# Kernel tuning notes

Hardware: AMD Instinct MI355X
Metric: run time of the kernel (lower is better)

## Reference

```python
import jax, jax.numpy as jnp
import numpy as np

B, S, D, H = 4, 2048, 1024, 16
HD = D // H  # 64

def setup_inputs() -> dict:
    key = jax.random.key(0)
    ks = jax.random.split(key, 6)
    scale = 1.0 / np.sqrt(D)
    return {
        "x": jax.random.normal(ks[0], (B, S, D), dtype=jnp.float32),
        "Wq": jax.random.normal(ks[1], (D, D), dtype=jnp.float32) * scale,
        "Wk": jax.random.normal(ks[2], (D, D), dtype=jnp.float32) * scale,
        "Wv": jax.random.normal(ks[3], (D, D), dtype=jnp.float32) * scale,
        "Wo": jax.random.normal(ks[4], (D, D), dtype=jnp.float32) * scale,
        "bo": jnp.zeros((D,), dtype=jnp.float32),
    }

def reference(x, Wq, Wk, Wv, Wo, bo):
    b, s, d = x.shape
    # projections (no bias for q/k/v, matching QKV_BIAS=False)
    q = (x @ Wq).reshape(b, s, H, HD).transpose(0, 2, 1, 3)  # [b,h,s,hd]
    k = (x @ Wk).reshape(b, s, H, HD).transpose(0, 2, 1, 3)
    v = (x @ Wv).reshape(b, s, H, HD).transpose(0, 2, 1, 3)
    scores = jnp.einsum('bhqd,bhkd->bhqk', q, k)  # [b,h,s,s]
    causal = jnp.tril(jnp.ones((s, s), dtype=bool))  # True where allowed
    scores = jnp.where(causal, scores, -jnp.inf)
    attn = jax.nn.softmax(scores / np.sqrt(HD), axis=-1)
    ctx = jnp.einsum('bhqk,bhkd->bhqd', attn, v)  # [b,h,s,hd]
    ctx = ctx.transpose(0, 2, 1, 3).reshape(b, s, d)
    return ctx @ Wo + bo
```

## Files before the change

kernel.cpp:

```cpp
#include <hip/hip_runtime.h>

#define BSZ 4
#define SEQ 2048
#define DIM 1024
#define NH  16
#define HD  64
#define QT  128
#define KT  64
#define PAD 72
#define NKT (DIM / 64)

typedef float v4f __attribute__((ext_vector_type(4)));
typedef short s8v __attribute__((ext_vector_type(8)));
typedef unsigned short u16;
typedef unsigned short u16x8 __attribute__((ext_vector_type(8)));
typedef unsigned short u16x4 __attribute__((ext_vector_type(4)));
typedef unsigned int u32;
typedef unsigned int u32x2 __attribute__((ext_vector_type(2)));
typedef unsigned int u32x4 __attribute__((ext_vector_type(4)));

__device__ __forceinline__ u16 f2bf(float f) {
  u32 u = __builtin_bit_cast(u32, f);
  u32 r = u + 0x7fffu + ((u >> 16) & 1u);
  return (u16)(r >> 16);
}
__device__ __forceinline__ u32 cvtpk(float lo, float hi) {
  u32 r; asm("v_cvt_pk_bf16_f32 %0, %1, %2" : "=v"(r) : "v"(lo), "v"(hi)); return r;
}
__device__ __forceinline__ u16 f2bf1(float f) { return (u16)cvtpk(f, f); }
__device__ __forceinline__ float fast_exp2(float x) {
#if __has_builtin(__builtin_amdgcn_exp2f)
  return __builtin_amdgcn_exp2f(x);
#else
  return exp2f(x);
#endif
}
__device__ __forceinline__ void gll16(const u16* g, u16* l) {
  __builtin_amdgcn_global_load_lds((const __attribute__((address_space(1))) void*)g,
                                   (__attribute__((address_space(3))) void*)l, 16, 0, 0);
}
__device__ __forceinline__ void wg_barrier() { asm volatile("s_barrier" ::: "memory"); }
#define WAITCNT_LGKM0 0xC07F
#define VMW6 __builtin_amdgcn_s_waitcnt(0xF76);
#define VMW0 __builtin_amdgcn_s_waitcnt(0xF70);

__global__ __launch_bounds__(256) void cast_bf16_kernel(const float* __restrict__ x,
                                                        u16* __restrict__ o, int n4) {
  int i = blockIdx.x * 256 + threadIdx.x;
  if (i >= n4) return;
  v4f v = reinterpret_cast<const v4f*>(x)[i];
  u16x4 r;
  #pragma unroll
  for (int c = 0; c < 4; c++) r[c] = f2bf(v[c]);
  reinterpret_cast<u16x4*>(o)[i] = r;
}

__global__ __launch_bounds__(256) void transpose_cast_kernel(const float* __restrict__ W0,
                                                             const float* __restrict__ W1,
                                                             const float* __restrict__ W2,
                                                             const float* __restrict__ W3,
                                                             u16* __restrict__ out) {
  const float* W = blockIdx.z == 0 ? W0 : blockIdx.z == 1 ? W1 : blockIdx.z == 2 ? W2 : W3;
  const float scale = (blockIdx.z == 0) ? 0.18033688011112042f : 1.0f;
  u16* T = out + (size_t)blockIdx.z * DIM * DIM;
  __shared__ float tile[32][33];
  int tx = threadIdx.x & 31, ty = threadIdx.x >> 5;
  int bn = blockIdx.x * 32, bk = blockIdx.y * 32;
  #pragma unroll
  for (int r = 0; r < 4; r++) {
    int k = bk + ty + r * 8;
    tile[ty + r * 8][tx] = W[(size_t)k * DIM + bn + tx];
  }
  __syncthreads();
  #pragma unroll
  for (int r = 0; r < 4; r++) {
    int n = bn + ty + r * 8;
    T[(size_t)n * DIM + bk + tx] = f2bf(tile[tx][ty + r * 8] * scale);
  }
}


#define ST_TILE(t_, s_)                                                           \
  gll16(Ag0 + (t_) * 64,      AW0 + (s_) * 16384);                                \
  gll16(Ag1 + (t_) * 64,      AW1 + (s_) * 16384);                                \
  gll16(Ag0 + (t_) * 64 + 32, AW0 + (s_) * 16384 + 8192);                         \
  gll16(Ag1 + (t_) * 64 + 32, AW1 + (s_) * 16384 + 8192);                         \
  gll16(Bg0 + (t_) * 64,      BW0 + (s_) * 8192);                                 \
  gll16(Bg0 + (t_) * 64 + 32, BW0 + (s_) * 8192 + 4096);

#define PH(t_, s_, STAGES, VMW)                                                   \
  { const u16* Ab = AL + (s_) * 16384 + aRd;                                      \
    const u16* Bb = BL + (s_) * 8192 + bRd;                                       \
    s8v af[2][4], bf[2][4];                                                       \
    _Pragma("unroll") for (int kc_ = 0; kc_ < 2; kc_++) {                         \
      _Pragma("unroll") for (int i_ = 0; i_ < 4; i_++)                            \
        af[kc_][i_] = *(const s8v*)(Ab + kc_ * 8192 + i_ * 512);                  \
      _Pragma("unroll") for (int j_ = 0; j_ < 4; j_++)                            \
        bf[kc_][j_] = *(const s8v*)(Bb + kc_ * 4096 + j_ * 512);                  \
    }                                                                             \
    STAGES                                                                        \
    VMW                                                                           \
    wg_barrier();                                                                 \
    __builtin_amdgcn_s_waitcnt(WAITCNT_LGKM0);                                    \
    __builtin_amdgcn_s_setprio(1);                                                \
    _Pragma("unroll") for (int kc_ = 0; kc_ < 2; kc_++)                           \
      _Pragma("unroll") for (int i_ = 0; i_ < 4; i_++)                            \
        _Pragma("unroll") for (int j_ = 0; j_ < 4; j_++)                          \
          acc[i_][j_] = __builtin_amdgcn_mfma_f32_16x16x32_bf16(                  \
              af[kc_][i_], bf[kc_][j_], acc[i_][j_], 0, 0, 0);                    \
    __builtin_amdgcn_s_setprio(0);                                                \
    wg_barrier(); }

#define GEMM256x128_CORE()                                                        \
  extern __shared__ __align__(16) u16 lds[];                                      \
  const int t = threadIdx.x;                                                      \
  const int lane = t & 63, w = t >> 6;                                            \
  const int waveM = w >> 1, waveN = w & 1;                                        \
  const int quad = lane >> 4, l16 = lane & 15;                                    \
  const int sR = lane & 15, sC = lane >> 4;                                       \
  u16* AL = lds;                                                                  \
  u16* BL = lds + 49152;                                                          \
  v4f acc[4][4];                                                                  \
  _Pragma("unroll") for (int i = 0; i < 4; i++)                                   \
    _Pragma("unroll") for (int j = 0; j < 4; j++)                                 \
      acc[i][j] = (v4f){0.f, 0.f, 0.f, 0.f};                                      \
  const u16* Ag0 = A + (size_t)(m0 + w * 32 + sR) * DIM + sC * 8;                 \
  const u16* Ag1 = Ag0 + 16 * DIM;                                                \
  const u16* Bg0 = Bt + (size_t)(n0 + w * 16 + sR) * DIM + sC * 8;                \
  u16* AW0 = AL + w * 1024;                                                       \
  u16* AW1 = AL + w * 1024 + 512;                                                 \
  u16* BW0 = BL + w * 512;                                                        \
  const int aRd = waveM * 2048 + quad * 128 + l16 * 8;                            \
  const int bRd = waveN * 2048 + quad * 128 + l16 * 8;                            \
  ST_TILE(0, 0) ST_TILE(1, 1)                                                     \
  VMW6                                                                            \
  wg_barrier();                                                                   \
  _Pragma("unroll") for (int t3 = 0; t3 < 12; t3 += 3) {                          \
    PH(t3 + 0, 0, ST_TILE(t3 + 2, 2), VMW6)                                       \
    PH(t3 + 1, 1, ST_TILE(t3 + 3, 0), VMW6)                                       \
    PH(t3 + 2, 2, ST_TILE(t3 + 4, 1), VMW6)                                       \
  }                                                                               \
  PH(12, 0, ST_TILE(14, 2), VMW6)                                                 \
  PH(13, 1, ST_TILE(15, 0), VMW6)                                                 \
  PH(14, 2, , VMW0)                                                               \
  PH(15, 0, , )

__global__ __launch_bounds__(512, 2) void gemm_qkv(const u16* __restrict__ A, const u16* __restrict__ Wt,
                                                   u16* __restrict__ Qb, u16* __restrict__ Kb,
                                                   u16* __restrict__ Vtg) {
  const int bid = blockIdx.x;
  const int swz = (bid & 7) * 96 + (bid >> 3);
  const int z = swz >> 8;
  const int rem = swz & 255;
  const int m0 = (rem >> 3) * 256;
  const int n0 = (rem & 7) * 128;
  const u16* Bt = Wt + (size_t)z * DIM * DIM;
  GEMM256x128_CORE()
  if (z == 2) {
    #pragma unroll
    for (int mi = 0; mi < 4; mi++) {
      #pragma unroll
      for (int ni = 0; ni < 4; ni++) {
        int gm0 = m0 + waveM * 64 + mi * 16 + quad * 4;
        int gn = n0 + waveN * 64 + ni * 16 + l16;
        int b = gm0 >> 11, s0 = gm0 & (SEQ - 1), hh = gn >> 6, d = gn & (HD - 1);
        u32x2 pw;
        pw[0] = cvtpk(acc[mi][ni][0], acc[mi][ni][1]);
        pw[1] = cvtpk(acc[mi][ni][2], acc[mi][ni][3]);
        *(u16x4*)(Vtg + ((size_t)(b * NH + hh) * HD + d) * SEQ + s0) =
            __builtin_bit_cast(u16x4, pw);
      }
    }
  } else {
    u16* C = (z == 0) ? Qb : Kb;
    #pragma unroll
    for (int mi = 0; mi < 4; mi++) {
      #pragma unroll
      for (int ni = 0; ni < 4; ni++) {
        int gn = n0 + waveN * 64 + ni * 16 + l16;
        #pragma unroll
        for (int r = 0; r < 4; r++) {
          int gm = m0 + waveM * 64 + mi * 16 + quad * 4 + r;
          C[(size_t)gm * DIM + gn] = f2bf1(acc[mi][ni][r]);
        }
      }
    }
  }
}

__global__ __launch_bounds__(512, 2) void gemm_proj(const u16* __restrict__ A, const u16* __restrict__ Bt,
                                                    float* __restrict__ Cf, const float* __restrict__ bias) {
  const int bid = blockIdx.x;
  const int swz = (bid & 7) * 32 + (bid >> 3);
  const int m0 = (swz >> 3) * 256;
  const int n0 = (swz & 7) * 128;
  GEMM256x128_CORE()
  #pragma unroll
  for (int ni = 0; ni < 4; ni++) {
    int gn = n0 + waveN * 64 + ni * 16 + l16;
    float bv = bias[gn];
    #pragma unroll
    for (int mi = 0; mi < 4; mi++) {
      #pragma unroll
      for (int r = 0; r < 4; r++) {
        int gm = m0 + waveM * 64 + mi * 16 + quad * 4 + r;
        Cf[(size_t)gm * DIM + gn] = acc[mi][ni][r] + bv;
      }
    }
  }
}

__global__ __launch_bounds__(256, 3) void flash_attn_mfma(const u16* __restrict__ Qb,
                                                          const u16* __restrict__ Kb,
                                                          const u16* __restrict__ Vtg,
                                                          u16* __restrict__ Ob) {
  const int h = blockIdx.x, px = blockIdx.y, bb = blockIdx.z;
  const int t = threadIdx.x;
  const int lane = t & 63, w = t >> 6;
  const int quad = lane >> 4, l16 = lane & 15;

  __shared__ u16 QPs[QT * PAD];
  __shared__ u16 Ks[KT * PAD];
  __shared__ u16 Vs[HD * PAD];

  const size_t qkbase = (size_t)bb * SEQ * DIM + h * HD;
  const size_t vbase = ((size_t)bb * NH + h) * (size_t)HD * SEQ;

  const int vrow = t >> 2, scol = (t & 3) * 16;
  const int krow = ((vrow >> 5) + 2 * ((vrow >> 2) & 1)) * 16 + ((vrow >> 3) & 3) * 4 + (vrow & 3);

  for (int pass = 0; pass < 2; pass++) {
    const int qi = (pass == 0) ? px : (SEQ / QT - 1 - px);
    const int q0 = qi * QT;
    const int wq = q0 + w * 32;
    const int ntiles = 2 * qi + 2;

    __syncthreads();

    {
      const int r = t >> 1, c0 = (t & 1) * 32;
      const u16* src = Qb + qkbase + (size_t)(q0 + r) * DIM + c0;
      #pragma unroll
      for (int ch = 0; ch < 4; ch++)
        *(u16x8*)(QPs + r * PAD + c0 + ch * 8) = *(const u16x8*)(src + ch * 8);
    }
    __syncthreads();

    s8v qf[2][2];
    #pragma unroll
    for (int ni = 0; ni < 2; ni++)
      #pragma unroll
      for (int kc = 0; kc < 2; kc++)
        qf[ni][kc] = *(const s8v*)(QPs + (w * 32 + ni * 16 + l16) * PAD + kc * 32 + quad * 8);

    u16x8 kr0, kr1, vr0, vr1;
    {
      const u16* kp = Kb + qkbase + (size_t)vrow * DIM + scol;
      kr0 = *(const u16x8*)kp; kr1 = *(const u16x8*)(kp + 8);
      const u16* vp = Vtg + vbase + (size_t)vrow * SEQ + scol;
      vr0 = *(const u16x8*)vp; vr1 = *(const u16x8*)(vp + 8);
    }

    float mrun[2] = {-1e30f, -1e30f}, lrun[2] = {0.f, 0.f};
    v4f O[4][2];
    #pragma unroll
    for (int di = 0; di < 4; di++)
      #pragma unroll
      for (int ni = 0; ni < 2; ni++) O[di][ni] = (v4f){0.f, 0.f, 0.f, 0.f};

    for (int it = 0; it < ntiles; ++it) {
      const int kv0 = it * KT;
      __syncthreads();
      *(u16x8*)(Ks + krow * PAD + scol) = kr0;
      *(u16x8*)(Ks + krow * PAD + scol + 8) = kr1;
      *(u16x8*)(Vs + vrow * PAD + scol) = vr0;
      *(u16x8*)(Vs + vrow * PAD + scol + 8) = vr1;
      __syncthreads();
      if (it + 1 < ntiles) {
        const int nkv = kv0 + KT;
        const u16* kp = Kb + qkbase + (size_t)(nkv + vrow) * DIM + scol;
        kr0 = *(const u16x8*)kp; kr1 = *(const u16x8*)(kp + 8);
        const u16* vp = Vtg + vbase + (size_t)vrow * SEQ + nkv + scol;
        vr0 = *(const u16x8*)vp; vr1 = *(const u16x8*)(vp + 8);
      }
      if (kv0 > wq + 31) continue;

      v4f sc[4][2];
      #pragma unroll
      for (int mi = 0; mi < 4; mi++)
        #pragma unroll
        for (int ni = 0; ni < 2; ni++) sc[mi][ni] = (v4f){0.f, 0.f, 0.f, 0.f};
      #pragma unroll
      for (int kc = 0; kc < 2; kc++) {
        #pragma unroll
        for (int mi = 0; mi < 4; mi++) {
          s8v kf = *(const s8v*)(Ks + (mi * 16 + l16) * PAD + kc * 32 + quad * 8);
          sc[mi][0] = __builtin_amdgcn_mfma_f32_16x16x32_bf16(kf, qf[0][kc], sc[mi][0], 0, 0, 0);
          sc[mi][1] = __builtin_amdgcn_mfma_f32_16x16x32_bf16(kf, qf[1][kc], sc[mi][1], 0, 0, 0);
        }
      }

      if (kv0 + KT > wq) {
        #pragma unroll
        for (int mi = 0; mi < 4; mi++) {
          const int kvb = kv0 + (mi & 1) * 32 + quad * 8 + (mi >> 1) * 4;
          #pragma unroll
          for (int ni = 0; ni < 2; ni++) {
            const int qg = wq + ni * 16 + l16;
            #pragma unroll
            for (int r = 0; r < 4; r++)
              if (kvb + r > qg) sc[mi][ni][r] = -1e30f;
          }
        }
      }

      float mx[2];
      #pragma unroll
      for (int ni = 0; ni < 2; ni++) {
        float m = -1e30f;
        #pragma unroll
        for (int mi = 0; mi < 4; mi++)
          #pragma unroll
          for (int r = 0; r < 4; r++) m = fmaxf(m, sc[mi][ni][r]);
        m = fmaxf(m, __shfl_xor(m, 16, 64));
        m = fmaxf(m, __shfl_xor(m, 32, 64));
        mx[ni] = m;
      }
      const bool defer = __all((mx[0] <= mrun[0] + 8.f) && (mx[1] <= mrun[1] + 8.f));
      if (!defer) {
        float alpha[2];
        #pragma unroll
        for (int ni = 0; ni < 2; ni++) {
          const float mnew = fmaxf(mrun[ni], mx[ni]);
          alpha[ni] = fast_exp2(mrun[ni] - mnew);
          mrun[ni] = mnew;
          lrun[ni] *= alpha[ni];
        }
        #pragma unroll
        for (int di = 0; di < 4; di++)
          #pragma unroll
          for (int ni = 0; ni < 2; ni++)
            #pragma unroll
            for (int r = 0; r < 4; r++) O[di][ni][r] *= alpha[ni];
      }
      #pragma unroll
      for (int ni = 0; ni < 2; ni++) {
        float rsum = 0.f;
        #pragma unroll
        for (int mi = 0; mi < 4; mi++)
          #pragma unroll
          for (int r = 0; r < 4; r++) {
            float p = fast_exp2(sc[mi][ni][r] - mrun[ni]);
            sc[mi][ni][r] = p;
            rsum += p;
          }
        rsum += __shfl_xor(rsum, 16, 64);
        rsum += __shfl_xor(rsum, 32, 64);
        lrun[ni] += rsum;
      }

      s8v pf[2][2];
      #pragma unroll
      for (int ni = 0; ni < 2; ni++)
        #pragma unroll
        for (int kc = 0; kc < 2; kc++) {
          u32x4 wds;
          wds[0] = cvtpk(sc[kc][ni][0], sc[kc][ni][1]);
          wds[1] = cvtpk(sc[kc][ni][2], sc[kc][ni][3]);
          wds[2] = cvtpk(sc[kc + 2][ni][0], sc[kc + 2][ni][1]);
          wds[3] = cvtpk(sc[kc + 2][ni][2], sc[kc + 2][ni][3]);
          pf[ni][kc] = __builtin_bit_cast(s8v, wds);
        }

      #pragma unroll
      for (int kc = 0; kc < 2; kc++) {
        #pragma unroll
        for (int di = 0; di < 4; di++) {
          s8v vf = *(const s8v*)(Vs + (di * 16 + l16) * PAD + kc * 32 + quad * 8);
          O[di][0] = __builtin_amdgcn_mfma_f32_16x16x32_bf16(vf, pf[0][kc], O[di][0], 0, 0, 0);
          O[di][1] = __builtin_amdgcn_mfma_f32_16x16x32_bf16(vf, pf[1][kc], O[di][1], 0, 0, 0);
        }
      }
    }

    const float inv0 = 1.f / lrun[0], inv1 = 1.f / lrun[1];
    #pragma unroll
    for (int di = 0; di < 4; di++)
      #pragma unroll
      for (int ni = 0; ni < 2; ni++) {
        const float inv = ni ? inv1 : inv0;
        #pragma unroll
        for (int r = 0; r < 4; r++)
          QPs[(w * 32 + ni * 16 + l16) * PAD + di * 16 + quad * 4 + r] = f2bf1(O[di][ni][r] * inv);
      }
    __syncthreads();
    {
      const int r = t >> 1, c0 = (t & 1) * 32;
      u16* dst = Ob + qkbase + (size_t)(q0 + r) * DIM + c0;
      #pragma unroll
      for (int ch = 0; ch < 4; ch++)
        *(u16x8*)(dst + ch * 8) = *(const u16x8*)(QPs + r * PAD + c0 + ch * 8);
    }
  }
}

extern "C" void kernel_launch(void* const* d_in, const int* in_sizes, int n_in,
                              void* d_out, int out_size, void* d_ws, size_t ws_size,
                              hipStream_t stream) {
  (void)in_sizes; (void)n_in; (void)out_size; (void)ws_size;
  const float* x  = (const float*)d_in[0];
  const float* Wq = (const float*)d_in[1];
  const float* Wk = (const float*)d_in[2];
  const float* Wv = (const float*)d_in[3];
  const float* Wo = (const float*)d_in[4];
  const float* bo = (const float*)d_in[5];
  float* out = (float*)d_out;

  static bool lds_attr_done = false;
  if (!lds_attr_done) {
    hipFuncSetAttribute(reinterpret_cast<const void*>(gemm_qkv),
                        hipFuncAttributeMaxDynamicSharedMemorySize, 147456);
    hipFuncSetAttribute(reinterpret_cast<const void*>(gemm_proj),
                        hipFuncAttributeMaxDynamicSharedMemorySize, 147456);
    lds_attr_done = true;
  }

  char* ws = (char*)d_ws;
  const size_t MB = 1024ull * 1024ull;
  u16* Xb  = (u16*)(ws);
  u16* Wt  = (u16*)(ws + 16 * MB);
  u16* Qb  = (u16*)(ws + 24 * MB);
  u16* Kb  = (u16*)(ws + 40 * MB);
  u16* Vtg = (u16*)(ws + 56 * MB);
  u16* Cb  = (u16*)(ws + 72 * MB);

  const int NTOK = BSZ * SEQ;
  const int n4 = NTOK * DIM / 4;
  cast_bf16_kernel<<<(n4 + 255) / 256, 256, 0, stream>>>(x, Xb, n4);
  transpose_cast_kernel<<<dim3(32, 32, 4), 256, 0, stream>>>(Wq, Wk, Wv, Wo, Wt);

  gemm_qkv<<<dim3(768), 512, 147456, stream>>>(Xb, Wt, Qb, Kb, Vtg);

  flash_attn_mfma<<<dim3(NH, SEQ / QT / 2, BSZ), 256, 0, stream>>>(Qb, Kb, Vtg, Cb);

  gemm_proj<<<dim3(256), 512, 147456, stream>>>(Cb, Wt + 3ull * DIM * DIM, out, bo);
}
```

Before: 266.2 us.

## Software-pipeline LDS fragment loads with MFMA in GEMM core via half-k double buffering

Restructures the GEMM main loop so each 64-wide k tile is split into two halves with separate register fragment sets (A/B). LDS reads for the next half are issued before the MFMAs on the current half run, with partial lgkmcnt waits and scheduling barriers. Global-to-LDS staging for the next tile also overlaps with compute, and the loop uses one barrier per tile instead of two. The cost is more live fragment registers, which could affect occupancy under the 512x2 launch bounds, plus a VMW0 wait each tile that may expose global load latency.

```diff
diff --git a/kernel.cpp b/kernel.cpp
--- a/kernel.cpp
+++ b/kernel.cpp
@@ -41,8 +41,10 @@
 }
 __device__ __forceinline__ void wg_barrier() { asm volatile("s_barrier" ::: "memory"); }
 #define WAITCNT_LGKM0 0xC07F
+#define WAITCNT_LGKM8 0xC87F
 #define VMW6 __builtin_amdgcn_s_waitcnt(0xF76);
 #define VMW0 __builtin_amdgcn_s_waitcnt(0xF70);
+#define SCHEDB __builtin_amdgcn_sched_barrier(0);
 
 __global__ __launch_bounds__(256) void cast_bf16_kernel(const float* __restrict__ x,
                                                         u16* __restrict__ o, int n4) {
@@ -88,28 +90,38 @@
   gll16(Bg0 + (t_) * 64,      BW0 + (s_) * 8192);                                 \
   gll16(Bg0 + (t_) * 64 + 32, BW0 + (s_) * 8192 + 4096);
 
-#define PH(t_, s_, STAGES, VMW)                                                   \
-  { const u16* Ab = AL + (s_) * 16384 + aRd;                                      \
-    const u16* Bb = BL + (s_) * 8192 + bRd;                                       \
-    s8v af[2][4], bf[2][4];                                                       \
-    _Pragma("unroll") for (int kc_ = 0; kc_ < 2; kc_++) {                         \
-      _Pragma("unroll") for (int i_ = 0; i_ < 4; i_++)                            \
-        af[kc_][i_] = *(const s8v*)(Ab + kc_ * 8192 + i_ * 512);                  \
-      _Pragma("unroll") for (int j_ = 0; j_ < 4; j_++)                            \
-        bf[kc_][j_] = *(const s8v*)(Bb + kc_ * 4096 + j_ * 512);                  \
-    }                                                                             \
-    STAGES                                                                        \
-    VMW                                                                           \
-    wg_barrier();                                                                 \
-    __builtin_amdgcn_s_waitcnt(WAITCNT_LGKM0);                                    \
-    __builtin_amdgcn_s_setprio(1);                                                \
-    _Pragma("unroll") for (int kc_ = 0; kc_ < 2; kc_++)                           \
-      _Pragma("unroll") for (int i_ = 0; i_ < 4; i_++)                            \
-        _Pragma("unroll") for (int j_ = 0; j_ < 4; j_++)                          \
-          acc[i_][j_] = __builtin_amdgcn_mfma_f32_16x16x32_bf16(                  \
-              af[kc_][i_], bf[kc_][j_], acc[i_][j_], 0, 0, 0);                    \
-    __builtin_amdgcn_s_setprio(0);                                                \
-    wg_barrier(); }
+#define MM(AF, BF)                                                                \
+  __builtin_amdgcn_s_setprio(1);                                                  \
+  _Pragma("unroll") for (int i_ = 0; i_ < 4; i_++)                                \
+    _Pragma("unroll") for (int j_ = 0; j_ < 4; j_++)                              \
+      acc[i_][j_] = __builtin_amdgcn_mfma_f32_16x16x32_bf16(                      \
+          AF[i_], BF[j_], acc[i_][j_], 0, 0, 0);                                  \
+  __builtin_amdgcn_s_setprio(0);
+
+#define PHA(s_)                                                                   \
+  _Pragma("unroll") for (int i_ = 0; i_ < 4; i_++)                                \
+    afB[i_] = *(const s8v*)(AL + (s_) * 16384 + 8192 + aRd + i_ * 512);           \
+  _Pragma("unroll") for (int j_ = 0; j_ < 4; j_++)                                \
+    bfB[j_] = *(const s8v*)(BL + (s_) * 8192 + 4096 + bRd + j_ * 512);            \
+  SCHEDB                                                                          \
+  __builtin_amdgcn_s_waitcnt(WAITCNT_LGKM8);                                      \
+  SCHEDB                                                                          \
+  MM(afA, bfA)                                                                    \
+  SCHEDB
+
+#define PHB(sn_, STG)                                                             \
+  VMW0                                                                            \
+  wg_barrier();                                                                   \
+  _Pragma("unroll") for (int i_ = 0; i_ < 4; i_++)                                \
+    afA[i_] = *(const s8v*)(AL + (sn_) * 16384 + aRd + i_ * 512);                 \
+  _Pragma("unroll") for (int j_ = 0; j_ < 4; j_++)                                \
+    bfA[j_] = *(const s8v*)(BL + (sn_) * 8192 + bRd + j_ * 512);                  \
+  STG                                                                             \
+  SCHEDB                                                                          \
+  __builtin_amdgcn_s_waitcnt(WAITCNT_LGKM8);                                      \
+  SCHEDB                                                                          \
+  MM(afB, bfB)                                                                    \
+  SCHEDB
 
 #define GEMM256x128_CORE()                                                        \
   extern __shared__ __align__(16) u16 lds[];                                      \
@@ -132,18 +144,34 @@
   u16* BW0 = BL + w * 512;                                                        \
   const int aRd = waveM * 2048 + quad * 128 + l16 * 8;                            \
   const int bRd = waveN * 2048 + quad * 128 + l16 * 8;                            \
+  s8v afA[4], bfA[4], afB[4], bfB[4];                                             \
   ST_TILE(0, 0) ST_TILE(1, 1)                                                     \
   VMW6                                                                            \
   wg_barrier();                                                                   \
-  _Pragma("unroll") for (int t3 = 0; t3 < 12; t3 += 3) {                          \
-    PH(t3 + 0, 0, ST_TILE(t3 + 2, 2), VMW6)                                       \
-    PH(t3 + 1, 1, ST_TILE(t3 + 3, 0), VMW6)                                       \
-    PH(t3 + 2, 2, ST_TILE(t3 + 4, 1), VMW6)                                       \
-  }                                                                               \
-  PH(12, 0, ST_TILE(14, 2), VMW6)                                                 \
-  PH(13, 1, ST_TILE(15, 0), VMW6)                                                 \
-  PH(14, 2, , VMW0)                                                               \
-  PH(15, 0, , )
+  _Pragma("unroll") for (int i = 0; i < 4; i++)                                   \
+    afA[i] = *(const s8v*)(AL + aRd + i * 512);                                   \
+  _Pragma("unroll") for (int j = 0; j < 4; j++)                                   \
+    bfA[j] = *(const s8v*)(BL + bRd + j * 512);                                   \
+  SCHEDB                                                                          \
+  PHA(0)  PHB(1, ST_TILE(2, 2))                                                   \
+  PHA(1)  PHB(2, ST_TILE(3, 0))                                                   \
+  PHA(2)  PHB(0, ST_TILE(4, 1))                                                   \
+  PHA(0)  PHB(1, ST_TILE(5, 2))                                                   \
+  PHA(1)  PHB(2, ST_TILE(6, 0))                                                   \
+  PHA(2)  PHB(0, ST_TILE(7, 1))                                                   \
+  PHA(0)  PHB(1, ST_TILE(8, 2))                                                   \
+  PHA(1)  PHB(2, ST_TILE(9, 0))                                                   \
+  PHA(2)  PHB(0, ST_TILE(10, 1))                                                  \
+  PHA(0)  PHB(1, ST_TILE(11, 2))                                                  \
+  PHA(1)  PHB(2, ST_TILE(12, 0))                                                  \
+  PHA(2)  PHB(0, ST_TILE(13, 1))                                                  \
+  PHA(0)  PHB(1, ST_TILE(14, 2))                                                  \
+  PHA(1)  PHB(2, ST_TILE(15, 0))                                                  \
+  PHA(2)  PHB(0, )                                                                \
+  PHA(0)                                                                          \
+  __builtin_amdgcn_s_waitcnt(WAITCNT_LGKM0);                                      \
+  SCHEDB                                                                          \
+  MM(afB, bfB)
 
 __global__ __launch_bounds__(512, 2) void gemm_qkv(const u16* __restrict__ A, const u16* __restrict__ Wt,
                                                    u16* __restrict__ Qb, u16* __restrict__ Kb,
```

Measured after the change: 279.9 us. +5.2%, slower.

## Rewrite QKV GEMM with 256x256 tiles and finer-grained pipelined phases

Applied to the files above, without the earlier changes.

Replaces the 256x128 QKV projection GEMM with a 256x256 tile per block, which halves the grid to 384 blocks. Each wave now computes a 128x64 sub-tile with 8x4 accumulators. The main loop is split into half-K sub-phases that interleave LDS fragment reads, global-to-LDS staging and MFMA, using double-buffered 128 KB LDS and sched barriers. The larger tile raises arithmetic intensity and cuts redundant global loads. In exchange it doubles accumulator register pressure, and with fewer blocks the GPU may be less evenly loaded.

```diff
diff --git a/kernel.cpp b/kernel.cpp
--- a/kernel.cpp
+++ b/kernel.cpp
@@ -8,7 +8,6 @@
 #define QT  128
 #define KT  64
 #define PAD 72
-#define NKT (DIM / 64)
 
 typedef float v4f __attribute__((ext_vector_type(4)));
 typedef short s8v __attribute__((ext_vector_type(8)));
@@ -41,8 +40,11 @@
 }
 __device__ __forceinline__ void wg_barrier() { asm volatile("s_barrier" ::: "memory"); }
 #define WAITCNT_LGKM0 0xC07F
+#define VMW8 __builtin_amdgcn_s_waitcnt(0xF78);
 #define VMW6 __builtin_amdgcn_s_waitcnt(0xF76);
+#define VMW4 __builtin_amdgcn_s_waitcnt(0xF74);
 #define VMW0 __builtin_amdgcn_s_waitcnt(0xF70);
+#define SCHEDB __builtin_amdgcn_sched_barrier(0);
 
 __global__ __launch_bounds__(256) void cast_bf16_kernel(const float* __restrict__ x,
                                                         u16* __restrict__ o, int n4) {
@@ -79,6 +81,130 @@
   }
 }
 
+
+#define QST_A(t_, kc_, d_)                                                        \
+  gll16(AgLo + (t_) * 64 + (kc_) * 32, ALw + (d_) * 16384 + (kc_) * 8192);        \
+  gll16(AgHi + (t_) * 64 + (kc_) * 32, ALw + (d_) * 16384 + (kc_) * 8192 + 4096);
+#define QST_B(t_, kc_, d_)                                                        \
+  gll16(BgLo + (t_) * 64 + (kc_) * 32, BLw + (d_) * 16384 + (kc_) * 8192);        \
+  gll16(BgHi + (t_) * 64 + (kc_) * 32, BLw + (d_) * 16384 + (kc_) * 8192 + 4096);
+
+#define QRDB(d_, kc_)                                                             \
+  bfr[0] = *(const s8v*)(BL + (d_) * 16384 + (kc_) * 8192 + (wn * 4 + 0) * 512 + rdo); \
+  bfr[1] = *(const s8v*)(BL + (d_) * 16384 + (kc_) * 8192 + (wn * 4 + 1) * 512 + rdo); \
+  bfr[2] = *(const s8v*)(BL + (d_) * 16384 + (kc_) * 8192 + (wn * 4 + 2) * 512 + rdo); \
+  bfr[3] = *(const s8v*)(BL + (d_) * 16384 + (kc_) * 8192 + (wn * 4 + 3) * 512 + rdo);
+
+#define QPH(d_, kc_, mh_, RDB_, STG_, VMW_)                                       \
+  { _Pragma("unroll") for (int i_ = 0; i_ < 4; i_++)                              \
+      afr[i_] = *(const s8v*)(AL + (d_) * 16384 + (kc_) * 8192 +                  \
+                              (wm * 8 + (mh_) * 4 + i_) * 512 + rdo);             \
+    RDB_                                                                          \
+    STG_                                                                          \
+    SCHEDB                                                                        \
+    VMW_                                                                          \
+    wg_barrier();                                                                 \
+    __builtin_amdgcn_s_waitcnt(WAITCNT_LGKM0);                                    \
+    SCHEDB                                                                        \
+    __builtin_amdgcn_s_setprio(1);                                                \
+    _Pragma("unroll") for (int i_ = 0; i_ < 4; i_++)                              \
+      _Pragma("unroll") for (int j_ = 0; j_ < 4; j_++)                            \
+        acc[(mh_) * 4 + i_][j_] = __builtin_amdgcn_mfma_f32_16x16x32_bf16(        \
+            afr[i_], bfr[j_], acc[(mh_) * 4 + i_][j_], 0, 0, 0);                  \
+    __builtin_amdgcn_s_setprio(0);                                                \
+    wg_barrier(); }
+
+__global__ __launch_bounds__(512, 2) void gemm_qkv(const u16* __restrict__ A, const u16* __restrict__ Wt,
+                                                   u16* __restrict__ Qb, u16* __restrict__ Kb,
+                                                   u16* __restrict__ Vtg) {
+  const int bid = blockIdx.x;
+  const int swz = (bid & 7) * 48 + (bid >> 3);
+  const int z = swz >> 7;
+  const int rem = swz & 127;
+  const int m0 = (rem >> 2) * 256;
+  const int n0 = (rem & 3) * 256;
+  const u16* Bt = Wt + (size_t)z * DIM * DIM;
+
+  extern __shared__ __align__(16) u16 lds[];
+  const int t = threadIdx.x;
+  const int lane = t & 63, w = t >> 6;
+  const int wm = w >> 2, wn = w & 3;
+  const int quad = lane >> 4, l16 = lane & 15;
+  const int sR = lane & 15, sC = lane >> 4;
+  u16* AL = lds;
+  u16* BL = lds + 32768;
+  u16* ALw = AL + w * 512;
+  u16* BLw = BL + w * 512;
+  const int rdo = quad * 128 + l16 * 8;
+  const u16* AgLo = A + (size_t)(m0 + w * 16 + sR) * DIM + sC * 8;
+  const u16* AgHi = AgLo + (size_t)128 * DIM;
+  const u16* BgLo = Bt + (size_t)(n0 + w * 16 + sR) * DIM + sC * 8;
+  const u16* BgHi = BgLo + (size_t)128 * DIM;
+
+  v4f acc[8][4];
+  #pragma unroll
+  for (int i = 0; i < 8; i++)
+    #pragma unroll
+    for (int j = 0; j < 4; j++) acc[i][j] = (v4f){0.f, 0.f, 0.f, 0.f};
+  s8v afr[4], bfr[4];
+
+  QST_A(0, 0, 0) QST_B(0, 0, 0) QST_A(0, 1, 0) QST_B(0, 1, 0)
+  QST_A(1, 0, 1) QST_B(1, 0, 1)
+  SCHEDB
+  VMW8
+  wg_barrier();
+
+  for (int it = 0; it < 7; ++it) {
+    const int kt = it * 2;
+    QPH(0, 0, 0, QRDB(0, 0), QST_A(kt + 1, 1, 1), )
+    QPH(0, 0, 1, ,           QST_B(kt + 1, 1, 1), VMW6)
+    QPH(0, 1, 0, QRDB(0, 1), QST_A(kt + 2, 0, 0), )
+    QPH(0, 1, 1, ,           QST_B(kt + 2, 0, 0), VMW6)
+    QPH(1, 0, 0, QRDB(1, 0), QST_A(kt + 2, 1, 0), )
+    QPH(1, 0, 1, ,           QST_B(kt + 2, 1, 0), VMW6)
+    QPH(1, 1, 0, QRDB(1, 1), QST_A(kt + 3, 0, 1), )
+    QPH(1, 1, 1, ,           QST_B(kt + 3, 0, 1), VMW6)
+  }
+  QPH(0, 0, 0, QRDB(0, 0), QST_A(15, 1, 1), )
+  QPH(0, 0, 1, ,           QST_B(15, 1, 1), VMW6)
+  QPH(0, 1, 0, QRDB(0, 1), , )
+  QPH(0, 1, 1, ,           , VMW4)
+  QPH(1, 0, 0, QRDB(1, 0), , )
+  QPH(1, 0, 1, ,           , VMW0)
+  QPH(1, 1, 0, QRDB(1, 1), , )
+  QPH(1, 1, 1, ,           , )
+
+  if (z == 2) {
+    #pragma unroll
+    for (int mi = 0; mi < 8; mi++) {
+      #pragma unroll
+      for (int ni = 0; ni < 4; ni++) {
+        int gm0 = m0 + wm * 128 + mi * 16 + quad * 4;
+        int gn = n0 + wn * 64 + ni * 16 + l16;
+        int b = gm0 >> 11, s0 = gm0 & (SEQ - 1), hh = gn >> 6, d = gn & (HD - 1);
+        u32x2 pw;
+        pw[0] = cvtpk(acc[mi][ni][0], acc[mi][ni][1]);
+        pw[1] = cvtpk(acc[mi][ni][2], acc[mi][ni][3]);
+        *(u16x4*)(Vtg + ((size_t)(b * NH + hh) * HD + d) * SEQ + s0) =
+            __builtin_bit_cast(u16x4, pw);
+      }
+    }
+  } else {
+    u16* C = (z == 0) ? Qb : Kb;
+    #pragma unroll
+    for (int mi = 0; mi < 8; mi++) {
+      #pragma unroll
+      for (int ni = 0; ni < 4; ni++) {
+        int gn = n0 + wn * 64 + ni * 16 + l16;
+        #pragma unroll
+        for (int r = 0; r < 4; r++) {
+          int gm = m0 + wm * 128 + mi * 16 + quad * 4 + r;
+          C[(size_t)gm * DIM + gn] = f2bf1(acc[mi][ni][r]);
+        }
+      }
+    }
+  }
+}
 
 #define ST_TILE(t_, s_)                                                           \
   gll16(Ag0 + (t_) * 64,      AW0 + (s_) * 16384);                                \
@@ -111,90 +237,46 @@
     __builtin_amdgcn_s_setprio(0);                                                \
     wg_barrier(); }
 
-#define GEMM256x128_CORE()                                                        \
-  extern __shared__ __align__(16) u16 lds[];                                      \
-  const int t = threadIdx.x;                                                      \
-  const int lane = t & 63, w = t >> 6;                                            \
-  const int waveM = w >> 1, waveN = w & 1;                                        \
-  const int quad = lane >> 4, l16 = lane & 15;                                    \
-  const int sR = lane & 15, sC = lane >> 4;                                       \
-  u16* AL = lds;                                                                  \
-  u16* BL = lds + 49152;                                                          \
-  v4f acc[4][4];                                                                  \
-  _Pragma("unroll") for (int i = 0; i < 4; i++)                                   \
-    _Pragma("unroll") for (int j = 0; j < 4; j++)                                 \
-      acc[i][j] = (v4f){0.f, 0.f, 0.f, 0.f};                                      \
-  const u16* Ag0 = A + (size_t)(m0 + w * 32 + sR) * DIM + sC * 8;                 \
-  const u16* Ag1 = Ag0 + 16 * DIM;                                                \
-  const u16* Bg0 = Bt + (size_t)(n0 + w * 16 + sR) * DIM + sC * 8;                \
-  u16* AW0 = AL + w * 1024;                                                       \
-  u16* AW1 = AL + w * 1024 + 512;                                                 \
-  u16* BW0 = BL + w * 512;                                                        \
-  const int aRd = waveM * 2048 + quad * 128 + l16 * 8;                            \
-  const int bRd = waveN * 2048 + quad * 128 + l16 * 8;                            \
-  ST_TILE(0, 0) ST_TILE(1, 1)                                                     \
-  VMW6                                                                            \
-  wg_barrier();                                                                   \
-  _Pragma("unroll") for (int t3 = 0; t3 < 12; t3 += 3) {                          \
-    PH(t3 + 0, 0, ST_TILE(t3 + 2, 2), VMW6)                                       \
-    PH(t3 + 1, 1, ST_TILE(t3 + 3, 0), VMW6)                                       \
-    PH(t3 + 2, 2, ST_TILE(t3 + 4, 1), VMW6)                                       \
-  }                                                                               \
-  PH(12, 0, ST_TILE(14, 2), VMW6)                                                 \
-  PH(13, 1, ST_TILE(15, 0), VMW6)                                                 \
-  PH(14, 2, , VMW0)                                                               \
-  PH(15, 0, , )
-
-__global__ __launch_bounds__(512, 2) void gemm_qkv(const u16* __restrict__ A, const u16* __restrict__ Wt,
-                                                   u16* __restrict__ Qb, u16* __restrict__ Kb,
-                                                   u16* __restrict__ Vtg) {
-  const int bid = blockIdx.x;
-  const int swz = (bid & 7) * 96 + (bid >> 3);
-  const int z = swz >> 8;
-  const int rem = swz & 255;
-  const int m0 = (rem >> 3) * 256;
-  const int n0 = (rem & 7) * 128;
-  const u16* Bt = Wt + (size_t)z * DIM * DIM;
-  GEMM256x128_CORE()
-  if (z == 2) {
-    #pragma unroll
-    for (int mi = 0; mi < 4; mi++) {
-      #pragma unroll
-      for (int ni = 0; ni < 4; ni++) {
-        int gm0 = m0 + waveM * 64 + mi * 16 + quad * 4;
-        int gn = n0 + waveN * 64 + ni * 16 + l16;
-        int b = gm0 >> 11, s0 = gm0 & (SEQ - 1), hh = gn >> 6, d = gn & (HD - 1);
-        u32x2 pw;
-        pw[0] = cvtpk(acc[mi][ni][0], acc[mi][ni][1]);
-        pw[1] = cvtpk(acc[mi][ni][2], acc[mi][ni][3]);
-        *(u16x4*)(Vtg + ((size_t)(b * NH + hh) * HD + d) * SEQ + s0) =
-            __builtin_bit_cast(u16x4, pw);
-      }
-    }
-  } else {
-    u16* C = (z == 0) ? Qb : Kb;
-    #pragma unroll
-    for (int mi = 0; mi < 4; mi++) {
-      #pragma unroll
-      for (int ni = 0; ni < 4; ni++) {
-        int gn = n0 + waveN * 64 + ni * 16 + l16;
-        #pragma unroll
-        for (int r = 0; r < 4; r++) {
-          int gm = m0 + waveM * 64 + mi * 16 + quad * 4 + r;
-          C[(size_t)gm * DIM + gn] = f2bf1(acc[mi][ni][r]);
-        }
-      }
-    }
-  }
-}
-
 __global__ __launch_bounds__(512, 2) void gemm_proj(const u16* __restrict__ A, const u16* __restrict__ Bt,
                                                     float* __restrict__ Cf, const float* __restrict__ bias) {
   const int bid = blockIdx.x;
   const int swz = (bid & 7) * 32 + (bid >> 3);
   const int m0 = (swz >> 3) * 256;
   const int n0 = (swz & 7) * 128;
-  GEMM256x128_CORE()
+  extern __shared__ __align__(16) u16 lds[];
+  const int t = threadIdx.x;
+  const int lane = t & 63, w = t >> 6;
+  const int waveM = w >> 1, waveN = w & 1;
+  const int quad = lane >> 4, l16 = lane & 15;
+  const int sR = lane & 15, sC = lane >> 4;
+  u16* AL = lds;
+  u16* BL = lds + 49152;
+  v4f acc[4][4];
+  #pragma unroll
+  for (int i = 0; i < 4; i++)
+    #pragma unroll
+    for (int j = 0; j < 4; j++) acc[i][j] = (v4f){0.f, 0.f, 0.f, 0.f};
+  const u16* Ag0 = A + (size_t)(m0 + w * 32 + sR) * DIM + sC * 8;
+  const u16* Ag1 = Ag0 + 16 * DIM;
+  const u16* Bg0 = Bt + (size_t)(n0 + w * 16 + sR) * DIM + sC * 8;
+  u16* AW0 = AL + w * 1024;
+  u16* AW1 = AL + w * 1024 + 512;
+  u16* BW0 = BL + w * 512;
+  const int aRd = waveM * 2048 + quad * 128 + l16 * 8;
+  const int bRd = waveN * 2048 + quad * 128 + l16 * 8;
+  ST_TILE(0, 0) ST_TILE(1, 1)
+  VMW6
+  wg_barrier();
+  #pragma unroll
+  for (int t3 = 0; t3 < 12; t3 += 3) {
+    PH(t3 + 0, 0, ST_TILE(t3 + 2, 2), VMW6)
+    PH(t3 + 1, 1, ST_TILE(t3 + 3, 0), VMW6)
+    PH(t3 + 2, 2, ST_TILE(t3 + 4, 1), VMW6)
+  }
+  PH(12, 0, ST_TILE(14, 2), VMW6)
+  PH(13, 1, ST_TILE(15, 0), VMW6)
+  PH(14, 2, , VMW0)
+  PH(15, 0, , )
   #pragma unroll
   for (int ni = 0; ni < 4; ni++) {
     int gn = n0 + waveN * 64 + ni * 16 + l16;
@@ -419,7 +501,7 @@
   static bool lds_attr_done = false;
   if (!lds_attr_done) {
     hipFuncSetAttribute(reinterpret_cast<const void*>(gemm_qkv),
-                        hipFuncAttributeMaxDynamicSharedMemorySize, 147456);
+                        hipFuncAttributeMaxDynamicSharedMemorySize, 131072);
     hipFuncSetAttribute(reinterpret_cast<const void*>(gemm_proj),
                         hipFuncAttributeMaxDynamicSharedMemorySize, 147456);
     lds_attr_done = true;
@@ -439,7 +521,7 @@
   cast_bf16_kernel<<<(n4 + 255) / 256, 256, 0, stream>>>(x, Xb, n4);
   transpose_cast_kernel<<<dim3(32, 32, 4), 256, 0, stream>>>(Wq, Wk, Wv, Wo, Wt);
 
-  gemm_qkv<<<dim3(768), 512, 147456, stream>>>(Xb, Wt, Qb, Kb, Vtg);
+  gemm_qkv<<<dim3(384), 512, 131072, stream>>>(Xb, Wt, Qb, Kb, Vtg);
 
   flash_attn_mfma<<<dim3(NH, SEQ / QT / 2, BSZ), 256, 0, stream>>>(Qb, Kb, Vtg, Cb);
 
```

After: 266.6 us. No clear change (+0.2%).
